# Kernel tuning notes

Measured on AMD Instinct MI355X. Metric: run time of the kernel, lower is better.

## Reference

```python
import jax, jax.numpy as jnp
import numpy as np

FP8_MAX = 448.0  # float8_e4m3fn max representable magnitude


def _to_fp8(x):
    # round-to-nearest fp8_e4m3 simulation via dtype cast
    return jnp.clip(x, -FP8_MAX, FP8_MAX).astype(jnp.float8_e4m3fn).astype(jnp.float32)


def setup_inputs() -> dict:
    key = jax.random.key(0)
    ks = jax.random.split(key, 8)
    T, H, I, E, K = 4096, 2048, 4096, 8, 2

    x = jax.random.normal(ks[0], (T, H), dtype=jnp.float32)
    selected_experts = jax.random.randint(ks[1], (T, K), 0, E, dtype=jnp.int32)
    rw = jax.random.uniform(ks[2], (T, K), dtype=jnp.float32) + 1e-3
    routing_weights = rw / jnp.sum(rw, axis=-1, keepdims=True)

    # float master weights -> per-tensor fp8 quantized buffers + weight scales
    w1_f = jax.random.normal(ks[3], (E, 2 * I, H), dtype=jnp.float32) * 0.02
    w2_f = jax.random.normal(ks[4], (E, H, I), dtype=jnp.float32) * 0.02
    w1_wscale = jnp.max(jnp.abs(w1_f), axis=(1, 2)) / FP8_MAX  # [E]
    w2_wscale = jnp.max(jnp.abs(w2_f), axis=(1, 2)) / FP8_MAX
    w1 = _to_fp8(w1_f / w1_wscale[:, None, None])  # fp8 values stored as f32
    w2 = _to_fp8(w2_f / w2_wscale[:, None, None])

    # per-tensor activation input scales (amax-style calibration constants)
    w1_iscale = jnp.full((E,), 4.0 / FP8_MAX, dtype=jnp.float32)
    w2_iscale = jnp.full((E,), 8.0 / FP8_MAX, dtype=jnp.float32)

    return {
        "x": x,
        "selected_experts": selected_experts,
        "routing_weights": routing_weights,
        "w1": w1,
        "w2": w2,
        "w1_iscale": w1_iscale,
        "w2_iscale": w2_iscale,
        "w1_wscale": w1_wscale,
        "w2_wscale": w2_wscale,
    }


def _fp8_linear(x, w_fp8, iscale, wscale):
    xq = _to_fp8(x / iscale)  # [T, in]
    return (xq @ w_fp8.T) * (iscale * wscale)  # [T, out]


def reference(x, selected_experts, routing_weights, w1, w2,
              w1_iscale, w2_iscale, w1_wscale, w2_wscale):
    E = w1.shape[0]
    I = w2.shape[2]
    out = jnp.zeros_like(x)
    for e in range(E):  # fixed small expert loop
        # combined routing weight for this expert per token: [T]
        gate = jnp.sum(
            jnp.where(selected_experts == e, routing_weights, 0.0), axis=-1)
        h = _fp8_linear(x, w1[e], w1_iscale[e], w1_wscale[e])  # [T, 2I]
        g, u = h[:, :I], h[:, I:]
        a = jax.nn.silu(g) * u  # gated activation
        y = _fp8_linear(a, w2[e], w2_iscale[e], w2_wscale[e])  # [T, H]
        out = out + gate[:, None] * y
    return out
```

## Files before the change

kernel.cpp:

```cpp
#include <hip/hip_runtime.h>
#include <cstdint>
#include <cstddef>

#define T_TOK 4096
#define H_DIM 2048
#define I_DIM 4096
#define E_NUM 8
#define CAP_ROWS 9216

#define OFF_COUNTS   0
#define OFF_CURSOR   64
#define OFF_PADOFF   128
#define OFF_TOKIDX   1024
#define OFF_TOKGATE  (OFF_TOKIDX + CAP_ROWS*4)
#define OFF_XQ       ((size_t)(OFF_TOKGATE + CAP_ROWS*4))
#define XQ_BYTES     ((size_t)CAP_ROWS*H_DIM*2)
#define OFF_AQ       (OFF_XQ + XQ_BYTES)
#define AQ_BYTES     ((size_t)CAP_ROWS*I_DIM*2)
#define OFF_W1B      (OFF_AQ + AQ_BYTES)
#define W1B_BYTES    ((size_t)E_NUM*2*I_DIM*H_DIM*2)
#define OFF_W2B      (OFF_W1B + W1B_BYTES)

typedef __bf16 bf16x8 __attribute__((ext_vector_type(8)));
typedef float  f32x4  __attribute__((ext_vector_type(4)));

__device__ __forceinline__ unsigned short bf16hi(float f) {
  return (unsigned short)(__float_as_uint(f) >> 16);
}

__device__ __forceinline__ float fp8_round(float v) {
  v = fminf(448.f, fmaxf(-448.f, v));
  float av = fabsf(v);
  if (av < 0.015625f) {
    return rintf(v * 512.f) * (1.f / 512.f);
  }
  unsigned u = __float_as_uint(v);
  unsigned lsb = (u >> 20) & 1u;
  u += 0x7FFFFu + lsb;
  u &= 0xFFF00000u;
  return __uint_as_float(u);
}

__device__ __forceinline__ void gld16(const void* g, void* l) {
  __builtin_amdgcn_global_load_lds(
      (__attribute__((address_space(1))) void*)((void*)g),
      (__attribute__((address_space(3))) void*)l, 16, 0, 0);
}

__global__ void k_count(const int* __restrict__ se, int* __restrict__ counts) {
  int t = blockIdx.x * 256 + threadIdx.x;
  if (t >= T_TOK) return;
  int e0 = se[t * 2], e1 = se[t * 2 + 1];
  atomicAdd(&counts[e0], 1);
  if (e1 != e0) atomicAdd(&counts[e1], 1);
}

__global__ void k_offsets(const int* __restrict__ counts, int* __restrict__ padOff) {
  if (threadIdx.x == 0 && blockIdx.x == 0) {
    int acc = 0;
    for (int e = 0; e < E_NUM; e++) {
      padOff[e] = acc;
      acc += ((counts[e] + 127) / 128) * 128;
    }
    padOff[E_NUM] = acc;
  }
}

__global__ void k_fill(const int* __restrict__ se, const float* __restrict__ rw,
                       const int* __restrict__ padOff, int* __restrict__ cursor,
                       int* __restrict__ tokIdx, float* __restrict__ tokGate) {
  int t = blockIdx.x * 256 + threadIdx.x;
  if (t >= T_TOK) return;
  int e0 = se[t * 2], e1 = se[t * 2 + 1];
  float w0 = rw[t * 2], w1 = rw[t * 2 + 1];
  float g0 = w0 + (e1 == e0 ? w1 : 0.f);
  int s0 = atomicAdd(&cursor[e0], 1);
  tokIdx[padOff[e0] + s0] = t;
  tokGate[padOff[e0] + s0] = g0;
  if (e1 != e0) {
    int s1 = atomicAdd(&cursor[e1], 1);
    tokIdx[padOff[e1] + s1] = t;
    tokGate[padOff[e1] + s1] = w1;
  }
}

__global__ __launch_bounds__(256)
void k_gather(const float* __restrict__ x, const int* __restrict__ padOff,
              const int* __restrict__ counts, const int* __restrict__ tokIdx,
              const float* __restrict__ w1_is, unsigned short* __restrict__ xq) {
  const int rblk = blockIdx.x;
  const int total = padOff[E_NUM];
  if (rblk >= total) return;
  int e = 0;
  while (rblk >= padOff[e + 1]) e++;
  unsigned short* dst = xq + (size_t)rblk * H_DIM;
  const int c = threadIdx.x * 8;
  const int local = rblk - padOff[e];
  if (local >= counts[e]) {
    uint4 z = {0u, 0u, 0u, 0u};
    *(uint4*)(dst + c) = z;
    return;
  }
  const int tok = tokIdx[rblk];
  const float is = w1_is[e];
  const float* src = x + (size_t)tok * H_DIM + c;
  float4 v0 = *(const float4*)(src);
  float4 v1 = *(const float4*)(src + 4);
  float q0 = fp8_round(v0.x / is), q1 = fp8_round(v0.y / is);
  float q2 = fp8_round(v0.z / is), q3 = fp8_round(v0.w / is);
  float q4 = fp8_round(v1.x / is), q5 = fp8_round(v1.y / is);
  float q6 = fp8_round(v1.z / is), q7 = fp8_round(v1.w / is);
  uint4 o;
  o.x = (unsigned)bf16hi(q0) | ((unsigned)bf16hi(q1) << 16);
  o.y = (unsigned)bf16hi(q2) | ((unsigned)bf16hi(q3) << 16);
  o.z = (unsigned)bf16hi(q4) | ((unsigned)bf16hi(q5) << 16);
  o.w = (unsigned)bf16hi(q6) | ((unsigned)bf16hi(q7) << 16);
  *(uint4*)(dst + c) = o;
}

__global__ __launch_bounds__(256)
void k_wconv(const float* __restrict__ w, unsigned short* __restrict__ o, long n4) {
  long i = (long)blockIdx.x * 256 + threadIdx.x;
  if (i >= n4) return;
  float4 v = ((const float4*)w)[i];
  ushort4 r;
  r.x = bf16hi(v.x); r.y = bf16hi(v.y); r.z = bf16hi(v.z); r.w = bf16hi(v.w);
  ((ushort4*)o)[i] = r;
}

__global__ __launch_bounds__(512, 1)
void k_gemm1(const unsigned short* __restrict__ xq,
             const unsigned short* __restrict__ w1b,
             const int* __restrict__ padOff,
             const float* __restrict__ w1_is, const float* __restrict__ w1_ws,
             const float* __restrict__ w2_is,
             unsigned short* __restrict__ aq) {
  const int e = blockIdx.z;
  const int rbase = padOff[e];
  const int rows = padOff[e + 1] - rbase;
  const int mt = blockIdx.y;
  if (mt * 128 >= rows) return;
  const int nt = blockIdx.x;

  __shared__ __align__(16) unsigned short As[128 * 32];
  __shared__ __align__(16) unsigned short Bg[128 * 32];
  __shared__ __align__(16) unsigned short Bu[128 * 32];

  const int tid = threadIdx.x;
  const int lane = tid & 63;
  const int wave = tid >> 6;
  const int wm = wave >> 2, wn = wave & 3;
  const int lr = lane & 15, quad = lane >> 4;

  const int r = tid >> 2;
  const int kb = tid & 3;
  const unsigned short* pa = xq + (size_t)(rbase + mt * 128 + r) * H_DIM + kb * 8;
  const unsigned short* pg = w1b + ((size_t)e * 2 * I_DIM + nt * 128 + r) * H_DIM + kb * 8;
  const unsigned short* pu = pg + (size_t)I_DIM * H_DIM;
  unsigned short* la = As + tid * 8;
  unsigned short* lg = Bg + tid * 8;
  unsigned short* lu = Bu + tid * 8;

  f32x4 accg[4][2] = {};
  f32x4 accu[4][2] = {};

  for (int k0 = 0; k0 < H_DIM; k0 += 32) {
    gld16(pa + k0, la);
    gld16(pg + k0, lg);
    gld16(pu + k0, lu);
    __syncthreads();
    bf16x8 af[4], gf[2], uf[2];
#pragma unroll
    for (int i = 0; i < 4; i++)
      af[i] = *(const bf16x8*)(As + (wm * 64 + i * 16 + lr) * 32 + quad * 8);
#pragma unroll
    for (int j = 0; j < 2; j++) {
      gf[j] = *(const bf16x8*)(Bg + (wn * 32 + j * 16 + lr) * 32 + quad * 8);
      uf[j] = *(const bf16x8*)(Bu + (wn * 32 + j * 16 + lr) * 32 + quad * 8);
    }
#pragma unroll
    for (int i = 0; i < 4; i++)
#pragma unroll
      for (int j = 0; j < 2; j++) {
        accg[i][j] = __builtin_amdgcn_mfma_f32_16x16x32_bf16(af[i], gf[j], accg[i][j], 0, 0, 0);
        accu[i][j] = __builtin_amdgcn_mfma_f32_16x16x32_bf16(af[i], uf[j], accu[i][j], 0, 0, 0);
      }
    __syncthreads();
  }

  const float s1 = w1_is[e] * w1_ws[e];
  const float is2 = w2_is[e];
#pragma unroll
  for (int i = 0; i < 4; i++)
#pragma unroll
    for (int j = 0; j < 2; j++)
#pragma unroll
      for (int rr = 0; rr < 4; rr++) {
        const int row = wm * 64 + i * 16 + quad * 4 + rr;
        const int col = nt * 128 + wn * 32 + j * 16 + lr;
        float g = accg[i][j][rr] * s1;
        float u = accu[i][j][rr] * s1;
        float a = (g / (1.f + expf(-g))) * u;
        float q = fp8_round(a / is2);
        aq[(size_t)(rbase + mt * 128 + row) * I_DIM + col] = bf16hi(q);
      }
}

__global__ __launch_bounds__(512, 1)
void k_gemm2(const unsigned short* __restrict__ aq,
             const unsigned short* __restrict__ w2b,
             const int* __restrict__ padOff, const int* __restrict__ counts,
             const int* __restrict__ tokIdx, const float* __restrict__ tokGate,
             const float* __restrict__ w2_is, const float* __restrict__ w2_ws,
             float* __restrict__ out) {
  const int e = blockIdx.z;
  const int rbase = padOff[e];
  const int rows = padOff[e + 1] - rbase;
  const int mt = blockIdx.y;
  if (mt * 128 >= rows) return;
  const int nt = blockIdx.x;
  const int cnt = counts[e];

  __shared__ __align__(16) unsigned short As[128 * 32];
  __shared__ __align__(16) unsigned short Bs[128 * 32];
  __shared__ int sTok[128];
  __shared__ float sGate[128];

  const int tid = threadIdx.x;
  const int lane = tid & 63;
  const int wave = tid >> 6;
  const int wm = wave >> 2, wn = wave & 3;
  const int lr = lane & 15, quad = lane >> 4;

  if (tid < 128) {
    int rr = mt * 128 + tid;
    if (rr < cnt) { sTok[tid] = tokIdx[rbase + rr]; sGate[tid] = tokGate[rbase + rr]; }
    else          { sTok[tid] = -1;                 sGate[tid] = 0.f; }
  }

  const int r = tid >> 2;
  const int kb = tid & 3;
  const unsigned short* pa = aq + (size_t)(rbase + mt * 128 + r) * I_DIM + kb * 8;
  const unsigned short* pb = w2b + ((size_t)e * H_DIM + nt * 128 + r) * I_DIM + kb * 8;
  unsigned short* la = As + tid * 8;
  unsigned short* lb = Bs + tid * 8;

  f32x4 acc[4][2] = {};

  for (int k0 = 0; k0 < I_DIM; k0 += 32) {
    gld16(pa + k0, la);
    gld16(pb + k0, lb);
    __syncthreads();
    bf16x8 af[4], bf[2];
#pragma unroll
    for (int i = 0; i < 4; i++)
      af[i] = *(const bf16x8*)(As + (wm * 64 + i * 16 + lr) * 32 + quad * 8);
#pragma unroll
    for (int j = 0; j < 2; j++)
      bf[j] = *(const bf16x8*)(Bs + (wn * 32 + j * 16 + lr) * 32 + quad * 8);
#pragma unroll
    for (int i = 0; i < 4; i++)
#pragma unroll
      for (int j = 0; j < 2; j++)
        acc[i][j] = __builtin_amdgcn_mfma_f32_16x16x32_bf16(af[i], bf[j], acc[i][j], 0, 0, 0);
    __syncthreads();
  }

  const float s2 = w2_is[e] * w2_ws[e];
#pragma unroll
  for (int i = 0; i < 4; i++)
#pragma unroll
    for (int j = 0; j < 2; j++)
#pragma unroll
      for (int rr = 0; rr < 4; rr++) {
        const int row = wm * 64 + i * 16 + quad * 4 + rr;
        const int tk = sTok[row];
        if (tk >= 0) {
          const int col = nt * 128 + wn * 32 + j * 16 + lr;
          unsafeAtomicAdd(out + (size_t)tk * H_DIM + col, sGate[row] * s2 * acc[i][j][rr]);
        }
      }
}

extern "C" void kernel_launch(void* const* d_in, const int* in_sizes, int n_in,
                              void* d_out, int out_size, void* d_ws, size_t ws_size,
                              hipStream_t stream) {
  const float* x     = (const float*)d_in[0];
  const int*   se    = (const int*)d_in[1];
  const float* rw    = (const float*)d_in[2];
  const float* w1    = (const float*)d_in[3];
  const float* w2    = (const float*)d_in[4];
  const float* w1_is = (const float*)d_in[5];
  const float* w2_is = (const float*)d_in[6];
  const float* w1_ws = (const float*)d_in[7];
  const float* w2_ws = (const float*)d_in[8];
  float* out = (float*)d_out;
  char* ws = (char*)d_ws;

  int*   counts  = (int*)(ws + OFF_COUNTS);
  int*   cursor  = (int*)(ws + OFF_CURSOR);
  int*   padOff  = (int*)(ws + OFF_PADOFF);
  int*   tokIdx  = (int*)(ws + OFF_TOKIDX);
  float* tokGate = (float*)(ws + OFF_TOKGATE);
  unsigned short* xq  = (unsigned short*)(ws + OFF_XQ);
  unsigned short* aq  = (unsigned short*)(ws + OFF_AQ);
  unsigned short* w1b = (unsigned short*)(ws + OFF_W1B);
  unsigned short* w2b = (unsigned short*)(ws + OFF_W2B);

  hipMemsetAsync(ws, 0, 1024, stream);
  hipMemsetAsync(d_out, 0, (size_t)T_TOK * H_DIM * sizeof(float), stream);

  k_count  <<<16, 256, 0, stream>>>(se, counts);
  k_offsets<<<1, 1, 0, stream>>>(counts, padOff);
  k_fill   <<<16, 256, 0, stream>>>(se, rw, padOff, cursor, tokIdx, tokGate);
  k_gather <<<CAP_ROWS, 256, 0, stream>>>(x, padOff, counts, tokIdx, w1_is, xq);

  k_wconv<<<131072, 256, 0, stream>>>(w1, w1b, (long)E_NUM * 2 * I_DIM * H_DIM / 4);
  k_wconv<<< 65536, 256, 0, stream>>>(w2, w2b, (long)E_NUM * H_DIM * I_DIM / 4);

  dim3 g1(I_DIM / 128, 32, E_NUM);
  k_gemm1<<<g1, 512, 0, stream>>>(xq, w1b, padOff, w1_is, w1_ws, w2_is, aq);

  dim3 g2(H_DIM / 128, 32, E_NUM);
  k_gemm2<<<g2, 512, 0, stream>>>(aq, w2b, padOff, counts, tokIdx, tokGate, w2_is, w2_ws, out);
}
```

Baseline: 1.600 ms.

## Switch expert GEMMs to native FP8 MFMA with swizzled LDS and atomic-free combine

Weights and activations are now stored as 8-bit e4m3 bytes instead of bf16, and both GEMMs use the scaled 16x16x128 FP8 MFMA with an XOR-swizzled LDS layout and K-steps of 128. GEMM1 uses a smaller N tile, and both kernels raise launch bounds to allow more blocks per CU. The atomic scatter into the output is replaced by writing per-slot results to a buffer and summing each token's two slots in a separate combine kernel, which also removes the output memset. This halves weight and activation bandwidth and doubles MFMA throughput. In exchange it adds an extra fp32 intermediate buffer, another kernel pass, and a hand-written FP8 encoder whose exactness must match the reference rounding.

Result: slower. 4.313 ms (+169.5%).

```diff
diff --git a/kernel.cpp b/kernel.cpp
--- a/kernel.cpp
+++ b/kernel.cpp
@@ -13,20 +13,16 @@
 #define OFF_PADOFF   128
 #define OFF_TOKIDX   1024
 #define OFF_TOKGATE  (OFF_TOKIDX + CAP_ROWS*4)
-#define OFF_XQ       ((size_t)(OFF_TOKGATE + CAP_ROWS*4))
-#define XQ_BYTES     ((size_t)CAP_ROWS*H_DIM*2)
-#define OFF_AQ       (OFF_XQ + XQ_BYTES)
-#define AQ_BYTES     ((size_t)CAP_ROWS*I_DIM*2)
-#define OFF_W1B      (OFF_AQ + AQ_BYTES)
-#define W1B_BYTES    ((size_t)E_NUM*2*I_DIM*H_DIM*2)
-#define OFF_W2B      (OFF_W1B + W1B_BYTES)
-
-typedef __bf16 bf16x8 __attribute__((ext_vector_type(8)));
-typedef float  f32x4  __attribute__((ext_vector_type(4)));
-
-__device__ __forceinline__ unsigned short bf16hi(float f) {
-  return (unsigned short)(__float_as_uint(f) >> 16);
-}
+#define OFF_TOKSLOT  (OFF_TOKGATE + CAP_ROWS*4)
+#define OFF_XQ       ((size_t)131072)
+#define OFF_AQ       (OFF_XQ + (size_t)CAP_ROWS*H_DIM)
+#define OFF_YB       (OFF_AQ + (size_t)CAP_ROWS*I_DIM)
+#define OFF_W1Q      (OFF_YB + (size_t)CAP_ROWS*H_DIM*4)
+#define OFF_W2Q      (OFF_W1Q + (size_t)E_NUM*2*I_DIM*H_DIM)
+
+typedef int   i32x4 __attribute__((ext_vector_type(4)));
+typedef int   i32x8 __attribute__((ext_vector_type(8)));
+typedef float f32x4 __attribute__((ext_vector_type(4)));
 
 __device__ __forceinline__ float fp8_round(float v) {
   v = fminf(448.f, fmaxf(-448.f, v));
@@ -41,10 +37,31 @@
   return __uint_as_float(u);
 }
 
+__device__ __forceinline__ unsigned fp8_enc(float v) {
+  unsigned u = __float_as_uint(v);
+  unsigned s = (u >> 24) & 0x80u;
+  float av = fabsf(v);
+  if (av < 0.015625f) {
+    unsigned m = (unsigned)(av * 512.0f + 0.5f);
+    return s | m;
+  }
+  unsigned E = (u >> 23) & 0xFFu;
+  unsigned mant = (u >> 20) & 7u;
+  return s | ((E - 120u) << 3) | mant;
+}
+
 __device__ __forceinline__ void gld16(const void* g, void* l) {
   __builtin_amdgcn_global_load_lds(
       (__attribute__((address_space(1))) void*)((void*)g),
       (__attribute__((address_space(3))) void*)l, 16, 0, 0);
+}
+
+__device__ __forceinline__ i32x8 frag_ld(const unsigned char* tile, int rowIdx, int quad) {
+  const int s = rowIdx & 7;
+  const unsigned char* r = tile + rowIdx * 128;
+  i32x4 lo = *(const i32x4*)(r + (((quad * 2)     ^ s) * 16));
+  i32x4 hi = *(const i32x4*)(r + (((quad * 2 + 1) ^ s) * 16));
+  return __builtin_shufflevector(lo, hi, 0, 1, 2, 3, 4, 5, 6, 7);
 }
 
 __global__ void k_count(const int* __restrict__ se, int* __restrict__ counts) {
@@ -68,73 +85,69 @@
 
 __global__ void k_fill(const int* __restrict__ se, const float* __restrict__ rw,
                        const int* __restrict__ padOff, int* __restrict__ cursor,
-                       int* __restrict__ tokIdx, float* __restrict__ tokGate) {
+                       int* __restrict__ tokIdx, float* __restrict__ tokGate,
+                       int* __restrict__ tokSlot) {
   int t = blockIdx.x * 256 + threadIdx.x;
   if (t >= T_TOK) return;
   int e0 = se[t * 2], e1 = se[t * 2 + 1];
   float w0 = rw[t * 2], w1 = rw[t * 2 + 1];
   float g0 = w0 + (e1 == e0 ? w1 : 0.f);
   int s0 = atomicAdd(&cursor[e0], 1);
-  tokIdx[padOff[e0] + s0] = t;
-  tokGate[padOff[e0] + s0] = g0;
+  int r0 = padOff[e0] + s0;
+  tokIdx[r0] = t; tokGate[r0] = g0; tokSlot[t * 2] = r0;
   if (e1 != e0) {
     int s1 = atomicAdd(&cursor[e1], 1);
-    tokIdx[padOff[e1] + s1] = t;
-    tokGate[padOff[e1] + s1] = w1;
+    int r1 = padOff[e1] + s1;
+    tokIdx[r1] = t; tokGate[r1] = w1; tokSlot[t * 2 + 1] = r1;
+  } else {
+    tokSlot[t * 2 + 1] = -1;
   }
 }
 
 __global__ __launch_bounds__(256)
 void k_gather(const float* __restrict__ x, const int* __restrict__ padOff,
               const int* __restrict__ counts, const int* __restrict__ tokIdx,
-              const float* __restrict__ w1_is, unsigned short* __restrict__ xq) {
+              const float* __restrict__ w1_is, unsigned char* __restrict__ xq) {
   const int rblk = blockIdx.x;
-  const int total = padOff[E_NUM];
-  if (rblk >= total) return;
+  if (rblk >= padOff[E_NUM]) return;
   int e = 0;
   while (rblk >= padOff[e + 1]) e++;
-  unsigned short* dst = xq + (size_t)rblk * H_DIM;
-  const int c = threadIdx.x * 8;
+  unsigned char* dst = xq + (size_t)rblk * H_DIM + threadIdx.x * 8;
   const int local = rblk - padOff[e];
   if (local >= counts[e]) {
-    uint4 z = {0u, 0u, 0u, 0u};
-    *(uint4*)(dst + c) = z;
+    *(uint2*)dst = make_uint2(0u, 0u);
     return;
   }
   const int tok = tokIdx[rblk];
   const float is = w1_is[e];
-  const float* src = x + (size_t)tok * H_DIM + c;
+  const float* src = x + (size_t)tok * H_DIM + threadIdx.x * 8;
   float4 v0 = *(const float4*)(src);
   float4 v1 = *(const float4*)(src + 4);
-  float q0 = fp8_round(v0.x / is), q1 = fp8_round(v0.y / is);
-  float q2 = fp8_round(v0.z / is), q3 = fp8_round(v0.w / is);
-  float q4 = fp8_round(v1.x / is), q5 = fp8_round(v1.y / is);
-  float q6 = fp8_round(v1.z / is), q7 = fp8_round(v1.w / is);
-  uint4 o;
-  o.x = (unsigned)bf16hi(q0) | ((unsigned)bf16hi(q1) << 16);
-  o.y = (unsigned)bf16hi(q2) | ((unsigned)bf16hi(q3) << 16);
-  o.z = (unsigned)bf16hi(q4) | ((unsigned)bf16hi(q5) << 16);
-  o.w = (unsigned)bf16hi(q6) | ((unsigned)bf16hi(q7) << 16);
-  *(uint4*)(dst + c) = o;
+  unsigned lo = fp8_enc(fp8_round(v0.x / is)) | (fp8_enc(fp8_round(v0.y / is)) << 8) |
+                (fp8_enc(fp8_round(v0.z / is)) << 16) | (fp8_enc(fp8_round(v0.w / is)) << 24);
+  unsigned hi = fp8_enc(fp8_round(v1.x / is)) | (fp8_enc(fp8_round(v1.y / is)) << 8) |
+                (fp8_enc(fp8_round(v1.z / is)) << 16) | (fp8_enc(fp8_round(v1.w / is)) << 24);
+  *(uint2*)dst = make_uint2(lo, hi);
 }
 
 __global__ __launch_bounds__(256)
-void k_wconv(const float* __restrict__ w, unsigned short* __restrict__ o, long n4) {
+void k_wconv(const float* __restrict__ w, unsigned char* __restrict__ o, long n8) {
   long i = (long)blockIdx.x * 256 + threadIdx.x;
-  if (i >= n4) return;
-  float4 v = ((const float4*)w)[i];
-  ushort4 r;
-  r.x = bf16hi(v.x); r.y = bf16hi(v.y); r.z = bf16hi(v.z); r.w = bf16hi(v.w);
-  ((ushort4*)o)[i] = r;
-}
-
-__global__ __launch_bounds__(512, 1)
-void k_gemm1(const unsigned short* __restrict__ xq,
-             const unsigned short* __restrict__ w1b,
+  if (i >= n8) return;
+  float4 v0 = ((const float4*)w)[i * 2];
+  float4 v1 = ((const float4*)w)[i * 2 + 1];
+  unsigned lo = fp8_enc(v0.x) | (fp8_enc(v0.y) << 8) | (fp8_enc(v0.z) << 16) | (fp8_enc(v0.w) << 24);
+  unsigned hi = fp8_enc(v1.x) | (fp8_enc(v1.y) << 8) | (fp8_enc(v1.z) << 16) | (fp8_enc(v1.w) << 24);
+  ((uint2*)o)[i] = make_uint2(lo, hi);
+}
+
+__global__ __launch_bounds__(512, 4)
+void k_gemm1(const unsigned char* __restrict__ xq,
+             const unsigned char* __restrict__ w1q,
              const int* __restrict__ padOff,
              const float* __restrict__ w1_is, const float* __restrict__ w1_ws,
              const float* __restrict__ w2_is,
-             unsigned short* __restrict__ aq) {
+             unsigned char* __restrict__ aq) {
   const int e = blockIdx.z;
   const int rbase = padOff[e];
   const int rows = padOff[e + 1] - rbase;
@@ -142,48 +155,53 @@
   if (mt * 128 >= rows) return;
   const int nt = blockIdx.x;
 
-  __shared__ __align__(16) unsigned short As[128 * 32];
-  __shared__ __align__(16) unsigned short Bg[128 * 32];
-  __shared__ __align__(16) unsigned short Bu[128 * 32];
+  __shared__ __align__(16) unsigned char As[128 * 128];
+  __shared__ __align__(16) unsigned char Bg[64 * 128];
+  __shared__ __align__(16) unsigned char Bu[64 * 128];
 
   const int tid = threadIdx.x;
   const int lane = tid & 63;
   const int wave = tid >> 6;
-  const int wm = wave >> 2, wn = wave & 3;
+  const int wm = wave >> 1, wn = wave & 1;
   const int lr = lane & 15, quad = lane >> 4;
 
-  const int r = tid >> 2;
-  const int kb = tid & 3;
-  const unsigned short* pa = xq + (size_t)(rbase + mt * 128 + r) * H_DIM + kb * 8;
-  const unsigned short* pg = w1b + ((size_t)e * 2 * I_DIM + nt * 128 + r) * H_DIM + kb * 8;
-  const unsigned short* pu = pg + (size_t)I_DIM * H_DIM;
-  unsigned short* la = As + tid * 8;
-  unsigned short* lg = Bg + tid * 8;
-  unsigned short* lu = Bu + tid * 8;
-
-  f32x4 accg[4][2] = {};
-  f32x4 accu[4][2] = {};
-
-  for (int k0 = 0; k0 < H_DIM; k0 += 32) {
-    gld16(pa + k0, la);
-    gld16(pg + k0, lg);
-    gld16(pu + k0, lu);
+  const int pr0 = tid >> 3,          pc0 = (tid & 7) ^ (pr0 & 7);
+  const int pr1 = (512 + tid) >> 3,  pc1 = ((512 + tid) & 7) ^ (pr1 & 7);
+  const unsigned char* gA0 = xq + (size_t)(rbase + mt * 128 + pr0) * H_DIM + pc0 * 16;
+  const unsigned char* gA1 = xq + (size_t)(rbase + mt * 128 + pr1) * H_DIM + pc1 * 16;
+  const unsigned char* gBg = w1q + ((size_t)e * 2 * I_DIM + nt * 64 + pr0) * H_DIM + pc0 * 16;
+  const unsigned char* gBu = w1q + ((size_t)e * 2 * I_DIM + I_DIM + nt * 64 + pr0) * H_DIM + pc0 * 16;
+  unsigned char* lA0 = As + tid * 16;
+  unsigned char* lA1 = As + (512 + tid) * 16;
+  unsigned char* lBg = Bg + tid * 16;
+  unsigned char* lBu = Bu + tid * 16;
+
+  f32x4 accg[2][2] = {};
+  f32x4 accu[2][2] = {};
+
+  for (int k0 = 0; k0 < H_DIM; k0 += 128) {
+    gld16(gA0 + k0, lA0);
+    gld16(gA1 + k0, lA1);
+    gld16(gBg + k0, lBg);
+    gld16(gBu + k0, lBu);
     __syncthreads();
-    bf16x8 af[4], gf[2], uf[2];
-#pragma unroll
-    for (int i = 0; i < 4; i++)
-      af[i] = *(const bf16x8*)(As + (wm * 64 + i * 16 + lr) * 32 + quad * 8);
+    i32x8 af[2], gf[2], uf[2];
+#pragma unroll
+    for (int i = 0; i < 2; i++)
+      af[i] = frag_ld(As, wm * 32 + i * 16 + lr, quad);
 #pragma unroll
     for (int j = 0; j < 2; j++) {
-      gf[j] = *(const bf16x8*)(Bg + (wn * 32 + j * 16 + lr) * 32 + quad * 8);
-      uf[j] = *(const bf16x8*)(Bu + (wn * 32 + j * 16 + lr) * 32 + quad * 8);
+      gf[j] = frag_ld(Bg, wn * 32 + j * 16 + lr, quad);
+      uf[j] = frag_ld(Bu, wn * 32 + j * 16 + lr, quad);
     }
 #pragma unroll
-    for (int i = 0; i < 4; i++)
+    for (int i = 0; i < 2; i++)
 #pragma unroll
       for (int j = 0; j < 2; j++) {
-        accg[i][j] = __builtin_amdgcn_mfma_f32_16x16x32_bf16(af[i], gf[j], accg[i][j], 0, 0, 0);
-        accu[i][j] = __builtin_amdgcn_mfma_f32_16x16x32_bf16(af[i], uf[j], accu[i][j], 0, 0, 0);
+        accg[i][j] = __builtin_amdgcn_mfma_scale_f32_16x16x128_f8f6f4(
+            af[i], gf[j], accg[i][j], 0, 0, 0, 127, 0, 127);
+        accu[i][j] = __builtin_amdgcn_mfma_scale_f32_16x16x128_f8f6f4(
+            af[i], uf[j], accu[i][j], 0, 0, 0, 127, 0, 127);
       }
     __syncthreads();
   }
@@ -191,28 +209,28 @@
   const float s1 = w1_is[e] * w1_ws[e];
   const float is2 = w2_is[e];
 #pragma unroll
-  for (int i = 0; i < 4; i++)
+  for (int i = 0; i < 2; i++)
 #pragma unroll
     for (int j = 0; j < 2; j++)
 #pragma unroll
       for (int rr = 0; rr < 4; rr++) {
-        const int row = wm * 64 + i * 16 + quad * 4 + rr;
-        const int col = nt * 128 + wn * 32 + j * 16 + lr;
+        const int row = wm * 32 + i * 16 + quad * 4 + rr;
+        const int col = nt * 64 + wn * 32 + j * 16 + lr;
         float g = accg[i][j][rr] * s1;
         float u = accu[i][j][rr] * s1;
         float a = (g / (1.f + expf(-g))) * u;
-        float q = fp8_round(a / is2);
-        aq[(size_t)(rbase + mt * 128 + row) * I_DIM + col] = bf16hi(q);
+        aq[(size_t)(rbase + mt * 128 + row) * I_DIM + col] =
+            (unsigned char)fp8_enc(fp8_round(a / is2));
       }
 }
 
-__global__ __launch_bounds__(512, 1)
-void k_gemm2(const unsigned short* __restrict__ aq,
-             const unsigned short* __restrict__ w2b,
+__global__ __launch_bounds__(512, 4)
+void k_gemm2(const unsigned char* __restrict__ aq,
+             const unsigned char* __restrict__ w2q,
              const int* __restrict__ padOff, const int* __restrict__ counts,
-             const int* __restrict__ tokIdx, const float* __restrict__ tokGate,
+             const float* __restrict__ tokGate,
              const float* __restrict__ w2_is, const float* __restrict__ w2_ws,
-             float* __restrict__ out) {
+             float* __restrict__ yb) {
   const int e = blockIdx.z;
   const int rbase = padOff[e];
   const int rows = padOff[e + 1] - rbase;
@@ -221,9 +239,8 @@
   const int nt = blockIdx.x;
   const int cnt = counts[e];
 
-  __shared__ __align__(16) unsigned short As[128 * 32];
-  __shared__ __align__(16) unsigned short Bs[128 * 32];
-  __shared__ int sTok[128];
+  __shared__ __align__(16) unsigned char As[128 * 128];
+  __shared__ __align__(16) unsigned char Bs[128 * 128];
   __shared__ float sGate[128];
 
   const int tid = threadIdx.x;
@@ -234,35 +251,41 @@
 
   if (tid < 128) {
     int rr = mt * 128 + tid;
-    if (rr < cnt) { sTok[tid] = tokIdx[rbase + rr]; sGate[tid] = tokGate[rbase + rr]; }
-    else          { sTok[tid] = -1;                 sGate[tid] = 0.f; }
-  }
-
-  const int r = tid >> 2;
-  const int kb = tid & 3;
-  const unsigned short* pa = aq + (size_t)(rbase + mt * 128 + r) * I_DIM + kb * 8;
-  const unsigned short* pb = w2b + ((size_t)e * H_DIM + nt * 128 + r) * I_DIM + kb * 8;
-  unsigned short* la = As + tid * 8;
-  unsigned short* lb = Bs + tid * 8;
+    sGate[tid] = (rr < cnt) ? tokGate[rbase + rr] : 0.f;
+  }
+
+  const int pr0 = tid >> 3,          pc0 = (tid & 7) ^ (pr0 & 7);
+  const int pr1 = (512 + tid) >> 3,  pc1 = ((512 + tid) & 7) ^ (pr1 & 7);
+  const unsigned char* gA0 = aq + (size_t)(rbase + mt * 128 + pr0) * I_DIM + pc0 * 16;
+  const unsigned char* gA1 = aq + (size_t)(rbase + mt * 128 + pr1) * I_DIM + pc1 * 16;
+  const unsigned char* gB0 = w2q + ((size_t)e * H_DIM + nt * 128 + pr0) * I_DIM + pc0 * 16;
+  const unsigned char* gB1 = w2q + ((size_t)e * H_DIM + nt * 128 + pr1) * I_DIM + pc1 * 16;
+  unsigned char* lA0 = As + tid * 16;
+  unsigned char* lA1 = As + (512 + tid) * 16;
+  unsigned char* lB0 = Bs + tid * 16;
+  unsigned char* lB1 = Bs + (512 + tid) * 16;
 
   f32x4 acc[4][2] = {};
 
-  for (int k0 = 0; k0 < I_DIM; k0 += 32) {
-    gld16(pa + k0, la);
-    gld16(pb + k0, lb);
+  for (int k0 = 0; k0 < I_DIM; k0 += 128) {
+    gld16(gA0 + k0, lA0);
+    gld16(gA1 + k0, lA1);
+    gld16(gB0 + k0, lB0);
+    gld16(gB1 + k0, lB1);
     __syncthreads();
-    bf16x8 af[4], bf[2];
+    i32x8 af[4], bf[2];
 #pragma unroll
     for (int i = 0; i < 4; i++)
-      af[i] = *(const bf16x8*)(As + (wm * 64 + i * 16 + lr) * 32 + quad * 8);
+      af[i] = frag_ld(As, wm * 64 + i * 16 + lr, quad);
 #pragma unroll
     for (int j = 0; j < 2; j++)
-      bf[j] = *(const bf16x8*)(Bs + (wn * 32 + j * 16 + lr) * 32 + quad * 8);
+      bf[j] = frag_ld(Bs, wn * 32 + j * 16 + lr, quad);
 #pragma unroll
     for (int i = 0; i < 4; i++)
 #pragma unroll
       for (int j = 0; j < 2; j++)
-        acc[i][j] = __builtin_amdgcn_mfma_f32_16x16x32_bf16(af[i], bf[j], acc[i][j], 0, 0, 0);
+        acc[i][j] = __builtin_amdgcn_mfma_scale_f32_16x16x128_f8f6f4(
+            af[i], bf[j], acc[i][j], 0, 0, 0, 127, 0, 127);
     __syncthreads();
   }
 
@@ -274,12 +297,25 @@
 #pragma unroll
       for (int rr = 0; rr < 4; rr++) {
         const int row = wm * 64 + i * 16 + quad * 4 + rr;
-        const int tk = sTok[row];
-        if (tk >= 0) {
-          const int col = nt * 128 + wn * 32 + j * 16 + lr;
-          unsafeAtomicAdd(out + (size_t)tk * H_DIM + col, sGate[row] * s2 * acc[i][j][rr]);
-        }
+        const int col = nt * 128 + wn * 32 + j * 16 + lr;
+        yb[(size_t)(rbase + mt * 128 + row) * H_DIM + col] =
+            acc[i][j][rr] * s2 * sGate[row];
       }
+}
+
+__global__ __launch_bounds__(256)
+void k_combine(const float* __restrict__ yb, const int* __restrict__ tokSlot,
+               float* __restrict__ out) {
+  int idx = blockIdx.x * 256 + threadIdx.x;
+  int t = idx >> 9;
+  int c = (idx & 511) * 4;
+  int s0 = tokSlot[t * 2], s1 = tokSlot[t * 2 + 1];
+  float4 v = *(const float4*)(yb + (size_t)s0 * H_DIM + c);
+  if (s1 >= 0) {
+    float4 w = *(const float4*)(yb + (size_t)s1 * H_DIM + c);
+    v.x += w.x; v.y += w.y; v.z += w.z; v.w += w.w;
+  }
+  *(float4*)(out + (size_t)t * H_DIM + c) = v;
 }
 
 extern "C" void kernel_launch(void* const* d_in, const int* in_sizes, int n_in,
@@ -302,25 +338,28 @@
   int*   padOff  = (int*)(ws + OFF_PADOFF);
   int*   tokIdx  = (int*)(ws + OFF_TOKIDX);
   float* tokGate = (float*)(ws + OFF_TOKGATE);
-  unsigned short* xq  = (unsigned short*)(ws + OFF_XQ);
-  unsigned short* aq  = (unsigned short*)(ws + OFF_AQ);
-  unsigned short* w1b = (unsigned short*)(ws + OFF_W1B);
-  unsigned short* w2b = (unsigned short*)(ws + OFF_W2B);
+  int*   tokSlot = (int*)(ws + OFF_TOKSLOT);
+  unsigned char* xq  = (unsigned char*)(ws + OFF_XQ);
+  unsigned char* aq  = (unsigned char*)(ws + OFF_AQ);
+  float*         yb  = (float*)(ws + OFF_YB);
+  unsigned char* w1q = (unsigned char*)(ws + OFF_W1Q);
+  unsigned char* w2q = (unsigned char*)(ws + OFF_W2Q);
 
   hipMemsetAsync(ws, 0, 1024, stream);
-  hipMemsetAsync(d_out, 0, (size_t)T_TOK * H_DIM * sizeof(float), stream);
 
   k_count  <<<16, 256, 0, stream>>>(se, counts);
   k_offsets<<<1, 1, 0, stream>>>(counts, padOff);
-  k_fill   <<<16, 256, 0, stream>>>(se, rw, padOff, cursor, tokIdx, tokGate);
+  k_fill   <<<16, 256, 0, stream>>>(se, rw, padOff, cursor, tokIdx, tokGate, tokSlot);
   k_gather <<<CAP_ROWS, 256, 0, stream>>>(x, padOff, counts, tokIdx, w1_is, xq);
 
-  k_wconv<<<131072, 256, 0, stream>>>(w1, w1b, (long)E_NUM * 2 * I_DIM * H_DIM / 4);
-  k_wconv<<< 65536, 256, 0, stream>>>(w2, w2b, (long)E_NUM * H_DIM * I_DIM / 4);
-
-  dim3 g1(I_DIM / 128, 32, E_NUM);
-  k_gemm1<<<g1, 512, 0, stream>>>(xq, w1b, padOff, w1_is, w1_ws, w2_is, aq);
+  k_wconv<<<65536, 256, 0, stream>>>(w1, w1q, (long)E_NUM * 2 * I_DIM * H_DIM / 8);
+  k_wconv<<<32768, 256, 0, stream>>>(w2, w2q, (long)E_NUM * H_DIM * I_DIM / 8);
+
+  dim3 g1(I_DIM / 64, 32, E_NUM);
+  k_gemm1<<<g1, 512, 0, stream>>>(xq, w1q, padOff, w1_is, w1_ws, w2_is, aq);
 
   dim3 g2(H_DIM / 128, 32, E_NUM);
-  k_gemm2<<<g2, 512, 0, stream>>>(aq, w2b, padOff, counts, tokIdx, tokGate, w2_is, w2_ws, out);
-}
+  k_gemm2<<<g2, 512, 0, stream>>>(aq, w2q, padOff, counts, tokGate, w2_is, w2_ws, yb);
+
+  k_combine<<<(T_TOK * H_DIM / 4) / 256, 256, 0, stream>>>(yb, tokSlot, out);
+}
```
